# Kernel tuning notes

Measured on AMD Instinct MI355X. Metric: run time of the kernel, lower is better.

Reference implementation:

```python
import jax, jax.numpy as jnp
import numpy as np

LN_EPS = 1e-5


def _layer_norm(x, g, b):
    m = jnp.mean(x, axis=-1, keepdims=True)
    v = jnp.mean(jnp.square(x - m), axis=-1, keepdims=True)
    return (x - m) * jax.lax.rsqrt(v + LN_EPS) * g + b


def _transition(x, g, bln, w_sw, w_ss, w_sig, b_sig, w_scale, residual):
    # TransitionBlock, eval mode (dropout = identity)
    x_in = x
    x = _layer_norm(x, g, bln)
    b = jax.nn.silu(x @ w_sw.T) * (x @ w_ss.T)
    y = jax.nn.sigmoid(x @ w_sig.T + b_sig) * (b @ w_scale.T)
    return x_in + y if residual else y


def setup_inputs() -> dict:
    N, E = 1000000, 100000
    F_DIM, A_DIM, H_DIM, HEADS = 64, 128, 256, 4
    D_IN = F_DIM + A_DIM
    key = jax.random.key(0)
    ks = jax.random.split(key, 16)
    s = 0.02
    inp = {
        'v_equivariant': jax.random.normal(ks[0], (N, 3), jnp.float32),
        'v_atom_features': jax.random.normal(ks[1], (N, A_DIM), jnp.float32),
        'edge_group_idx': jnp.sort(jax.random.randint(ks[2], (N,), 0, E)).astype(jnp.int32),
        'num_edges': E,
        'fourier_w': jax.random.normal(ks[3], (F_DIM,), jnp.float32),
        'fourier_b': jax.random.normal(ks[4], (F_DIM,), jnp.float32),
        # TransitionBlock 1 (input 192 -> 256, no residual)
        'tb1_ln_g': jnp.ones((D_IN,), jnp.float32),
        'tb1_ln_b': jnp.zeros((D_IN,), jnp.float32),
        'tb1_w_sw': jax.random.normal(ks[5], (H_DIM, D_IN), jnp.float32) * s,
        'tb1_w_ss': jax.random.normal(ks[6], (H_DIM, D_IN), jnp.float32) * s,
        'tb1_w_sig': jax.random.normal(ks[7], (H_DIM, D_IN), jnp.float32) * s,
        'tb1_b_sig': jnp.full((H_DIM,), -2.0, jnp.float32),
        'tb1_w_scale': jax.random.normal(ks[8], (H_DIM, H_DIM), jnp.float32) * s,
        # TransitionBlock 2 (256 -> 256, residual)
        'tb2_ln_g': jnp.ones((H_DIM,), jnp.float32),
        'tb2_ln_b': jnp.zeros((H_DIM,), jnp.float32),
        'tb2_w_sw': jax.random.normal(ks[9], (H_DIM, H_DIM), jnp.float32) * s,
        'tb2_w_ss': jax.random.normal(ks[10], (H_DIM, H_DIM), jnp.float32) * s,
        'tb2_w_sig': jax.random.normal(ks[11], (H_DIM, H_DIM), jnp.float32) * s,
        'tb2_b_sig': jnp.full((H_DIM,), -2.0, jnp.float32),
        'tb2_w_scale': jax.random.normal(ks[12], (H_DIM, H_DIM), jnp.float32) * s,
        # final linear 256 -> num_heads
        'out_w': jax.random.normal(ks[13], (HEADS, H_DIM), jnp.float32) * s,
        'out_b': jnp.zeros((HEADS,), jnp.float32),
    }
    return inp


def reference(v_equivariant, v_atom_features, edge_group_idx, num_edges,
              fourier_w, fourier_b,
              tb1_ln_g, tb1_ln_b, tb1_w_sw, tb1_w_ss, tb1_w_sig, tb1_b_sig, tb1_w_scale,
              tb2_ln_g, tb2_ln_b, tb2_w_sw, tb2_w_ss, tb2_w_sig, tb2_b_sig, tb2_w_scale,
              out_w, out_b):
    # Fourier embedding of vector norms: [N] -> [N, F_DIM]
    v_norms = jnp.linalg.norm(v_equivariant, axis=-1)
    f_dist = jnp.cos(2.0 * jnp.pi * (v_norms[..., None] * fourier_w + fourier_b))
    x = jnp.concatenate([f_dist, v_atom_features], axis=-1)  # [N, 192]
    x = _transition(x, tb1_ln_g, tb1_ln_b, tb1_w_sw, tb1_w_ss, tb1_w_sig, tb1_b_sig, tb1_w_scale, residual=False)
    x = _transition(x, tb2_ln_g, tb2_ln_b, tb2_w_sw, tb2_w_ss, tb2_w_sig, tb2_b_sig, tb2_w_scale, residual=True)
    scores = x @ out_w.T + out_b  # [N, H]
    # scatter_softmax over edge groups (per head)
    smax = jax.ops.segment_max(scores, edge_group_idx, num_segments=num_edges)
    e = jnp.exp(scores - smax[edge_group_idx])
    ssum = jax.ops.segment_sum(e, edge_group_idx, num_segments=num_edges)
    alphas = e / ssum[edge_group_idx]  # [N, H]
    # weighted scatter-sum pooling of 3-vectors per head
    v_weighted = v_equivariant[:, None, :] * alphas[..., None]  # [N, H, 3]
    v_pooled = jax.ops.segment_sum(v_weighted, edge_group_idx, num_segments=num_edges)
    return v_pooled.reshape(num_edges, -1)  # [E, H*3]
```

## Files before the change

kernel.cpp:

```cpp
#include <hip/hip_runtime.h>
#include <math.h>

#define DIN   192
#define HD    256
#define ROWS  64
#define THREADS 256
#define LSTR  256

typedef __bf16 bf16_t;
typedef bf16_t bf16x8 __attribute__((ext_vector_type(8)));
typedef unsigned short u16x8 __attribute__((ext_vector_type(8)));
typedef float  f32x16 __attribute__((ext_vector_type(16)));

static __device__ __forceinline__ f32x16 mfma32(bf16x8 a, bf16x8 b, f32x16 c) {
  return __builtin_amdgcn_mfma_f32_32x32x16_bf16(a, b, c, 0, 0, 0);
}
static __device__ __forceinline__ unsigned short f2bfu(float f) {
  bf16_t h = (bf16_t)f; unsigned short u; __builtin_memcpy(&u, &h, 2); return u;
}
static __device__ __forceinline__ float bfu2f(unsigned short u) {
  unsigned x = ((unsigned)u) << 16; float f; __builtin_memcpy(&f, &x, 4); return f;
}
static __device__ __forceinline__ unsigned pk2(float a, float b) {
  return (unsigned)f2bfu(a) | ((unsigned)f2bfu(b) << 16);
}
static __device__ __forceinline__ float lo16(unsigned u) { return bfu2f((unsigned short)(u & 0xffff)); }
static __device__ __forceinline__ float hi16(unsigned u) { return bfu2f((unsigned short)(u >> 16)); }
static __device__ __forceinline__ float sigm(float x) {
  return __builtin_amdgcn_rcpf(1.f + __expf(-x));
}
static __device__ __forceinline__ int lidx(int row, int col) {
  return row * LSTR + (col ^ ((row & 7) << 3));
}
static __device__ __forceinline__ int crow(int r, int kg) {
  return (r & 3) + 8 * (r >> 2) + 4 * kg;
}

#define OFF_WSW1 0
#define OFF_WSS1 49152
#define OFF_WSG1 98304
#define OFF_WSC1 147456
#define OFF_WSW2 212992
#define OFF_WSS2 278528
#define OFF_WSG2 344064
#define OFF_WSC2 409600
#define OFF_WOUT 475136
#define NGRP_REORD 59392
#define NGRP_ALL   60416

__global__ void iab_wconv_kernel(const float* __restrict__ a0, const float* __restrict__ a1,
                                 const float* __restrict__ a2, const float* __restrict__ a3,
                                 const float* __restrict__ a4, const float* __restrict__ a5,
                                 const float* __restrict__ a6, const float* __restrict__ a7,
                                 const float* __restrict__ a8, unsigned short* __restrict__ out)
{
  const int i = blockIdx.x * 256 + threadIdx.x;
  if (i >= NGRP_ALL) return;
  if (i >= NGRP_REORD) {
    const int g  = i - NGRP_REORD;
    const int ks = g >> 6;
    const int ln = g & 63;
    const int col = ln & 31;
    const int kg  = ln >> 5;
    #pragma unroll
    for (int j = 0; j < 8; ++j) {
      const float vv = (col < 4) ? a8[col * 256 + ks * 16 + kg * 8 + j] : 0.f;
      out[OFF_WOUT + (size_t)g * 8 + j] = f2bfu(vv);
    }
    return;
  }
  const float* src; int off, Kd, g;
  if      (i < 6144)  { src = a0; off = OFF_WSW1; Kd = 192; g = i; }
  else if (i < 12288) { src = a1; off = OFF_WSS1; Kd = 192; g = i - 6144; }
  else if (i < 18432) { src = a2; off = OFF_WSG1; Kd = 192; g = i - 12288; }
  else if (i < 26624) { src = a3; off = OFF_WSC1; Kd = 256; g = i - 18432; }
  else if (i < 34816) { src = a4; off = OFF_WSW2; Kd = 256; g = i - 26624; }
  else if (i < 43008) { src = a5; off = OFF_WSS2; Kd = 256; g = i - 34816; }
  else if (i < 51200) { src = a6; off = OFF_WSG2; Kd = 256; g = i - 43008; }
  else                { src = a7; off = OFF_WSC2; Kd = 256; g = i - 51200; }
  const int KS   = Kd >> 4;
  const int tile = g / (KS * 64);
  const int rem  = g - tile * (KS * 64);
  const int ks   = rem >> 6;
  const int ln   = rem & 63;
  const float* sp = src + (size_t)(tile * 32 + (ln & 31)) * Kd + ks * 16 + (ln >> 5) * 8;
  #pragma unroll
  for (int j = 0; j < 8; ++j) out[off + (size_t)g * 8 + j] = f2bfu(sp[j]);
}

template<int KS>
static __device__ __forceinline__ void bgphase(const unsigned short* __restrict__ Wsw,
                                               const unsigned short* __restrict__ Wss,
                                               const unsigned short* __restrict__ Wsg,
                                               const unsigned short* __restrict__ sIn,
                                               unsigned short* __restrict__ sOut,
                                               int l31, int kg, int xr, int ocol, float bias,
                                               unsigned (&sg0)[8], unsigned (&sg1)[8])
{
  f32x16 u0{}, u1{}, s0{}, s1{}, g0{}, g1{};
  #pragma unroll 2
  for (int ks = 0; ks < KS; ++ks) {
    const bf16x8 wa = *(const bf16x8*)(Wsw + ks * 512);
    const bf16x8 wb = *(const bf16x8*)(Wss + ks * 512);
    const bf16x8 wg = *(const bf16x8*)(Wsg + ks * 512);
    const int off = ((ks * 16) + kg * 8) ^ xr;
    const bf16x8 A0 = *(const bf16x8*)(sIn + l31 * LSTR + off);
    const bf16x8 A1 = *(const bf16x8*)(sIn + (32 + l31) * LSTR + off);
    u0 = mfma32(A0, wa, u0); u1 = mfma32(A1, wa, u1);
    s0 = mfma32(A0, wb, s0); s1 = mfma32(A1, wb, s1);
    g0 = mfma32(A0, wg, g0); g1 = mfma32(A1, wg, g1);
  }
  #pragma unroll
  for (int i = 0; i < 16; ++i) {
    const float x0 = u0[i];
    const float x1 = u1[i];
    sOut[lidx(crow(i, kg),      ocol)] = f2bfu(x0 * sigm(x0) * s0[i]);
    sOut[lidx(32 + crow(i, kg), ocol)] = f2bfu(x1 * sigm(x1) * s1[i]);
  }
  #pragma unroll
  for (int p = 0; p < 8; ++p) {
    sg0[p] = pk2(sigm(g0[2*p] + bias), sigm(g0[2*p+1] + bias));
    sg1[p] = pk2(sigm(g1[2*p] + bias), sigm(g1[2*p+1] + bias));
  }
}

template<int RES>
static __device__ __forceinline__ void scphase(const unsigned short* __restrict__ Wc,
                                               const unsigned short* __restrict__ sBin,
                                               unsigned short* __restrict__ sAout,
                                               int l31, int kg, int xr, int ocol,
                                               const unsigned (&sg0)[8], const unsigned (&sg1)[8],
                                               unsigned (&x0)[8], unsigned (&x1)[8])
{
  f32x16 c0{}, c1{};
  #pragma unroll 4
  for (int ks = 0; ks < 16; ++ks) {
    const bf16x8 wv = *(const bf16x8*)(Wc + ks * 512);
    const int off = ((ks * 16) + kg * 8) ^ xr;
    const bf16x8 A0 = *(const bf16x8*)(sBin + l31 * LSTR + off);
    const bf16x8 A1 = *(const bf16x8*)(sBin + (32 + l31) * LSTR + off);
    c0 = mfma32(A0, wv, c0);
    c1 = mfma32(A1, wv, c1);
  }
  #pragma unroll
  for (int p = 0; p < 8; ++p) {
    const float ya0 = lo16(sg0[p]) * c0[2*p],  ya1 = hi16(sg0[p]) * c0[2*p+1];
    const float yb0 = lo16(sg1[p]) * c1[2*p],  yb1 = hi16(sg1[p]) * c1[2*p+1];
    if (RES) {
      x0[p] = pk2(lo16(x0[p]) + ya0, hi16(x0[p]) + ya1);
      x1[p] = pk2(lo16(x1[p]) + yb0, hi16(x1[p]) + yb1);
    } else {
      x0[p] = pk2(ya0, ya1);
      x1[p] = pk2(yb0, yb1);
    }
    const int r0 = crow(2 * p, kg);
    sAout[lidx(r0,          ocol)] = (unsigned short)(x0[p] & 0xffff);
    sAout[lidx(r0 + 1,      ocol)] = (unsigned short)(x0[p] >> 16);
    sAout[lidx(32 + r0,     ocol)] = (unsigned short)(x1[p] & 0xffff);
    sAout[lidx(32 + r0 + 1, ocol)] = (unsigned short)(x1[p] >> 16);
  }
}

#define LNACC(P) { \
  float e_; \
  e_ = bfu2f(P[0]); s += e_; sq += e_ * e_; \
  e_ = bfu2f(P[1]); s += e_; sq += e_ * e_; \
  e_ = bfu2f(P[2]); s += e_; sq += e_ * e_; \
  e_ = bfu2f(P[3]); s += e_; sq += e_ * e_; \
  e_ = bfu2f(P[4]); s += e_; sq += e_ * e_; \
  e_ = bfu2f(P[5]); s += e_; sq += e_ * e_; \
  e_ = bfu2f(P[6]); s += e_; sq += e_ * e_; \
  e_ = bfu2f(P[7]); s += e_; sq += e_ * e_; }

#define LNNORM(P, GPTR, BPTR, BASE) { \
  const int base_ = (BASE); \
  const float4 ga_ = *(const float4*)((GPTR) + base_); \
  const float4 gb_ = *(const float4*)((GPTR) + base_ + 4); \
  const float4 oa_ = *(const float4*)((BPTR) + base_); \
  const float4 ob_ = *(const float4*)((BPTR) + base_ + 4); \
  u16x8 q_; \
  q_[0] = f2bfu((bfu2f(P[0]) - mean) * rstd * ga_.x + oa_.x); \
  q_[1] = f2bfu((bfu2f(P[1]) - mean) * rstd * ga_.y + oa_.y); \
  q_[2] = f2bfu((bfu2f(P[2]) - mean) * rstd * ga_.z + oa_.z); \
  q_[3] = f2bfu((bfu2f(P[3]) - mean) * rstd * ga_.w + oa_.w); \
  q_[4] = f2bfu((bfu2f(P[4]) - mean) * rstd * gb_.x + ob_.x); \
  q_[5] = f2bfu((bfu2f(P[5]) - mean) * rstd * gb_.y + ob_.y); \
  q_[6] = f2bfu((bfu2f(P[6]) - mean) * rstd * gb_.z + ob_.z); \
  q_[7] = f2bfu((bfu2f(P[7]) - mean) * rstd * gb_.w + ob_.w); \
  *(u16x8*)(sA + r * LSTR + (base_ ^ xrr)) = q_; }

__global__ __launch_bounds__(THREADS, 2)
void iab_rows_mfma(
    const float* __restrict__ v, const float* __restrict__ af,
    const float* __restrict__ fw, const float* __restrict__ fb,
    const float* __restrict__ ln1g, const float* __restrict__ ln1b,
    const float* __restrict__ bsig1,
    const float* __restrict__ ln2g, const float* __restrict__ ln2b,
    const float* __restrict__ bsig2,
    const float* __restrict__ outb,
    const unsigned short* __restrict__ wc,
    float* __restrict__ scores, int N)
{
  __shared__ __align__(16) unsigned short sA[ROWS * LSTR];
  __shared__ __align__(16) unsigned short sB[ROWS * LSTR];

  const int t    = threadIdx.x;
  const int w    = t >> 6;
  const int lane = t & 63;
  const int l31  = lane & 31;
  const int kg   = lane >> 5;
  const int xr   = (lane & 7) << 3;
  const int row0 = blockIdx.x * ROWS;
  const int oc0  = w * 64 + l31;
  const int oc1  = oc0 + 32;
  const int T0   = w * 2;
  const int T1   = w * 2 + 1;
  const int lb   = lane * 8;

  #pragma unroll 1
  for (int it = 0; it < 2; ++it) {
    const int r   = (t >> 3) + it * 32;
    const int sub = t & 7;
    const int g   = row0 + r;
    const int xrr = (r & 7) << 3;
    float s = 0.f, sq = 0.f;
    u16x8 p0, p1 = {}, p2 = {};
    {
      float vx = 0.f, vy = 0.f, vz = 0.f;
      if (g < N) {
        vx = v[3 * (size_t)g + 0];
        vy = v[3 * (size_t)g + 1];
        vz = v[3 * (size_t)g + 2];
      }
      const float nrm = sqrtf(vx * vx + vy * vy + vz * vz);
      const float4 fwa = *(const float4*)(fw + sub * 8);
      const float4 fwb = *(const float4*)(fw + sub * 8 + 4);
      const float4 fba = *(const float4*)(fb + sub * 8);
      const float4 fbb = *(const float4*)(fb + sub * 8 + 4);
      const float e0 = __cosf(6.283185307179586f * (nrm * fwa.x + fba.x));
      const float e1 = __cosf(6.283185307179586f * (nrm * fwa.y + fba.y));
      const float e2 = __cosf(6.283185307179586f * (nrm * fwa.z + fba.z));
      const float e3 = __cosf(6.283185307179586f * (nrm * fwa.w + fba.w));
      const float e4 = __cosf(6.283185307179586f * (nrm * fwb.x + fbb.x));
      const float e5 = __cosf(6.283185307179586f * (nrm * fwb.y + fbb.y));
      const float e6 = __cosf(6.283185307179586f * (nrm * fwb.z + fbb.z));
      const float e7 = __cosf(6.283185307179586f * (nrm * fwb.w + fbb.w));
      s  += e0 + e1 + e2 + e3 + e4 + e5 + e6 + e7;
      sq += e0*e0 + e1*e1 + e2*e2 + e3*e3 + e4*e4 + e5*e5 + e6*e6 + e7*e7;
      p0[0] = f2bfu(e0); p0[1] = f2bfu(e1); p0[2] = f2bfu(e2); p0[3] = f2bfu(e3);
      p0[4] = f2bfu(e4); p0[5] = f2bfu(e5); p0[6] = f2bfu(e6); p0[7] = f2bfu(e7);
    }
    if (g < N) {
      const float* ap = af + (size_t)g * 128 + sub * 8;
      {
        const float4 a0 = *(const float4*)(ap);
        const float4 a1 = *(const float4*)(ap + 4);
        s  += a0.x + a0.y + a0.z + a0.w + a1.x + a1.y + a1.z + a1.w;
        sq += a0.x*a0.x + a0.y*a0.y + a0.z*a0.z + a0.w*a0.w
            + a1.x*a1.x + a1.y*a1.y + a1.z*a1.z + a1.w*a1.w;
        p1[0] = f2bfu(a0.x); p1[1] = f2bfu(a0.y); p1[2] = f2bfu(a0.z); p1[3] = f2bfu(a0.w);
        p1[4] = f2bfu(a1.x); p1[5] = f2bfu(a1.y); p1[6] = f2bfu(a1.z); p1[7] = f2bfu(a1.w);
      }
      {
        const float4 a2 = *(const float4*)(ap + 64);
        const float4 a3 = *(const float4*)(ap + 68);
        s  += a2.x + a2.y + a2.z + a2.w + a3.x + a3.y + a3.z + a3.w;
        sq += a2.x*a2.x + a2.y*a2.y + a2.z*a2.z + a2.w*a2.w
            + a3.x*a3.x + a3.y*a3.y + a3.z*a3.z + a3.w*a3.w;
        p2[0] = f2bfu(a2.x); p2[1] = f2bfu(a2.y); p2[2] = f2bfu(a2.z); p2[3] = f2bfu(a2.w);
        p2[4] = f2bfu(a3.x); p2[5] = f2bfu(a3.y); p2[6] = f2bfu(a3.z); p2[7] = f2bfu(a3.w);
      }
    }
    #pragma unroll
    for (int o = 1; o < 8; o <<= 1) {
      s  += __shfl_xor(s,  o);
      sq += __shfl_xor(sq, o);
    }
    const float mean = s * (1.f / 192.f);
    const float var  = fmaxf(sq * (1.f / 192.f) - mean * mean, 0.f);
    const float rstd = rsqrtf(var + 1e-5f);
    LNNORM(p0, ln1g, ln1b, sub * 8);
    LNNORM(p1, ln1g, ln1b, 64 + sub * 8);
    LNNORM(p2, ln1g, ln1b, 128 + sub * 8);
  }
  __syncthreads();

  unsigned xT0M0[8], xT0M1[8], xT1M0[8], xT1M1[8];
  unsigned gT0M0[8], gT0M1[8], gT1M0[8], gT1M1[8];

  bgphase<12>(wc + OFF_WSW1 + T0 * 12 * 512 + lb,
              wc + OFF_WSS1 + T0 * 12 * 512 + lb,
              wc + OFF_WSG1 + T0 * 12 * 512 + lb,
              sA, sB, l31, kg, xr, oc0, bsig1[oc0], gT0M0, gT0M1);
  __builtin_amdgcn_sched_barrier(0);
  bgphase<12>(wc + OFF_WSW1 + T1 * 12 * 512 + lb,
              wc + OFF_WSS1 + T1 * 12 * 512 + lb,
              wc + OFF_WSG1 + T1 * 12 * 512 + lb,
              sA, sB, l31, kg, xr, oc1, bsig1[oc1], gT1M0, gT1M1);
  __syncthreads();

  scphase<0>(wc + OFF_WSC1 + T0 * 16 * 512 + lb, sB, sA,
             l31, kg, xr, oc0, gT0M0, gT0M1, xT0M0, xT0M1);
  __builtin_amdgcn_sched_barrier(0);
  scphase<0>(wc + OFF_WSC1 + T1 * 16 * 512 + lb, sB, sA,
             l31, kg, xr, oc1, gT1M0, gT1M1, xT1M0, xT1M1);
  __syncthreads();

  #pragma unroll 1
  for (int it = 0; it < 2; ++it) {
    const int r   = (t >> 3) + it * 32;
    const int sub = t & 7;
    const int xrr = (r & 7) << 3;
    const u16x8 rv0 = *(const u16x8*)(sA + r * LSTR + ((sub * 32 +  0) ^ xrr));
    const u16x8 rv1 = *(const u16x8*)(sA + r * LSTR + ((sub * 32 +  8) ^ xrr));
    const u16x8 rv2 = *(const u16x8*)(sA + r * LSTR + ((sub * 32 + 16) ^ xrr));
    const u16x8 rv3 = *(const u16x8*)(sA + r * LSTR + ((sub * 32 + 24) ^ xrr));
    float s = 0.f, sq = 0.f;
    LNACC(rv0);
    LNACC(rv1);
    LNACC(rv2);
    LNACC(rv3);
    #pragma unroll
    for (int o = 1; o < 8; o <<= 1) {
      s  += __shfl_xor(s,  o);
      sq += __shfl_xor(sq, o);
    }
    const float mean = s * (1.f / 256.f);
    const float var  = fmaxf(sq * (1.f / 256.f) - mean * mean, 0.f);
    const float rstd = rsqrtf(var + 1e-5f);
    LNNORM(rv0, ln2g, ln2b, sub * 32 +  0);
    LNNORM(rv1, ln2g, ln2b, sub * 32 +  8);
    LNNORM(rv2, ln2g, ln2b, sub * 32 + 16);
    LNNORM(rv3, ln2g, ln2b, sub * 32 + 24);
  }
  __syncthreads();

  bgphase<16>(wc + OFF_WSW2 + T0 * 16 * 512 + lb,
              wc + OFF_WSS2 + T0 * 16 * 512 + lb,
              wc + OFF_WSG2 + T0 * 16 * 512 + lb,
              sA, sB, l31, kg, xr, oc0, bsig2[oc0], gT0M0, gT0M1);
  __builtin_amdgcn_sched_barrier(0);
  bgphase<16>(wc + OFF_WSW2 + T1 * 16 * 512 + lb,
              wc + OFF_WSS2 + T1 * 16 * 512 + lb,
              wc + OFF_WSG2 + T1 * 16 * 512 + lb,
              sA, sB, l31, kg, xr, oc1, bsig2[oc1], gT1M0, gT1M1);
  __syncthreads();

  scphase<1>(wc + OFF_WSC2 + T0 * 16 * 512 + lb, sB, sA,
             l31, kg, xr, oc0, gT0M0, gT0M1, xT0M0, xT0M1);
  __builtin_amdgcn_sched_barrier(0);
  scphase<1>(wc + OFF_WSC2 + T1 * 16 * 512 + lb, sB, sA,
             l31, kg, xr, oc1, gT1M0, gT1M1, xT1M0, xT1M1);
  __syncthreads();

  if (w < 2) {
    const unsigned short* WtF = wc + OFF_WOUT + (size_t)lane * 8;
    f32x16 c{};
    #pragma unroll 4
    for (int ks = 0; ks < 16; ++ks) {
      const bf16x8 wf = *(const bf16x8*)(WtF + ks * 512);
      const bf16x8 A  = *(const bf16x8*)(sA + (w * 32 + l31) * LSTR + (((ks * 16) + kg * 8) ^ xr));
      c = mfma32(A, wf, c);
    }
    if (l31 < 4) {
      const float bias = outb[l31];
      #pragma unroll
      for (int i = 0; i < 16; ++i) {
        const int g = row0 + w * 32 + crow(i, kg);
        if (g < N) scores[(size_t)g * 4 + l31] = c[i] + bias;
      }
    }
  }
}

__device__ __forceinline__ int iab_lower_bound(const int* __restrict__ a, int n, int key)
{
  int lo = 0, hi = n;
  while (lo < hi) {
    const int mid = (lo + hi) >> 1;
    if (a[mid] < key) lo = mid + 1; else hi = mid;
  }
  return lo;
}

__global__ __launch_bounds__(256)
void iab_segpool_kernel(const float* __restrict__ scores,
                        const float* __restrict__ v,
                        const int* __restrict__ gidx,
                        float* __restrict__ out, int N, int E)
{
  const int seg  = blockIdx.x * 4 + (threadIdx.x >> 6);
  const int lane = threadIdx.x & 63;
  if (seg >= E) return;

  const int lo = iab_lower_bound(gidx, N, seg);
  const int hi = iab_lower_bound(gidx, N, seg + 1);

  const int h  = lane & 3;
  const int ro = lane >> 2;

  float m = -INFINITY;
  for (int base = lo; base < hi; base += 16) {
    const int r = base + ro;
    if (r < hi) m = fmaxf(m, scores[(size_t)r * 4 + h]);
  }
  #pragma unroll
  for (int o = 4; o < 64; o <<= 1) m = fmaxf(m, __shfl_xor(m, o));

  float ssum = 0.f, w0 = 0.f, w1 = 0.f, w2 = 0.f;
  for (int base = lo; base < hi; base += 16) {
    const int r = base + ro;
    if (r < hi) {
      const float e = expf(scores[(size_t)r * 4 + h] - m);
      ssum += e;
      w0 += e * v[3 * (size_t)r + 0];
      w1 += e * v[3 * (size_t)r + 1];
      w2 += e * v[3 * (size_t)r + 2];
    }
  }
  #pragma unroll
  for (int o = 4; o < 64; o <<= 1) {
    ssum += __shfl_xor(ssum, o);
    w0   += __shfl_xor(w0, o);
    w1   += __shfl_xor(w1, o);
    w2   += __shfl_xor(w2, o);
  }

  if (ro == 0) {
    const float inv = (hi > lo) ? (1.f / ssum) : 0.f;
    out[(size_t)seg * 12 + h * 3 + 0] = w0 * inv;
    out[(size_t)seg * 12 + h * 3 + 1] = w1 * inv;
    out[(size_t)seg * 12 + h * 3 + 2] = w2 * inv;
  }
}

extern "C" void kernel_launch(void* const* d_in, const int* in_sizes, int n_in,
                              void* d_out, int out_size, void* d_ws, size_t ws_size,
                              hipStream_t stream)
{
  const float* v     = (const float*)d_in[0];
  const float* af    = (const float*)d_in[1];
  const int*   gidx  = (const int*)  d_in[2];
  const float* fw    = (const float*)d_in[4];
  const float* fb    = (const float*)d_in[5];
  const float* ln1g  = (const float*)d_in[6];
  const float* ln1b  = (const float*)d_in[7];
  const float* wsw1  = (const float*)d_in[8];
  const float* wss1  = (const float*)d_in[9];
  const float* wsig1 = (const float*)d_in[10];
  const float* bsig1 = (const float*)d_in[11];
  const float* wsc1  = (const float*)d_in[12];
  const float* ln2g  = (const float*)d_in[13];
  const float* ln2b  = (const float*)d_in[14];
  const float* wsw2  = (const float*)d_in[15];
  const float* wss2  = (const float*)d_in[16];
  const float* wsig2 = (const float*)d_in[17];
  const float* bsig2 = (const float*)d_in[18];
  const float* wsc2  = (const float*)d_in[19];
  const float* outw  = (const float*)d_in[20];
  const float* outb  = (const float*)d_in[21];

  const int N = in_sizes[0] / 3;
  const int E = out_size / 12;

  float* scores = (float*)d_ws;
  unsigned short* wcv = (unsigned short*)((char*)d_ws + (size_t)N * 4 * sizeof(float));

  hipLaunchKernelGGL(iab_wconv_kernel, dim3((NGRP_ALL + 255) / 256), dim3(256), 0, stream,
                     wsw1, wss1, wsig1, wsc1, wsw2, wss2, wsig2, wsc2, outw, wcv);

  hipLaunchKernelGGL(iab_rows_mfma, dim3((N + ROWS - 1) / ROWS), dim3(THREADS), 0, stream,
                     v, af, fw, fb, ln1g, ln1b, bsig1, ln2g, ln2b, bsig2, outb,
                     wcv, scores, N);

  hipLaunchKernelGGL(iab_segpool_kernel, dim3((E + 3) / 4), dim3(256), 0, stream,
                     scores, v, gidx, (float*)d_out, N, E);
}
```

Baseline: 2.417 ms.

## Move sigmoid-gate GEMM from first phase into scale phase to cut live registers

The sigmoid-gate projection is taken out of the swish/linear phase and computed at the start of the scale phase instead, reading the LN input still held in sA. Results are kept in registers and written back to sA only after an extra barrier, because sA is now read during that phase. This shortens the first phase to four accumulators and drops the packed gate registers carried across phases, aiming to reduce register pressure and raise occupancy. The cost is an additional __syncthreads per transition block and a longer second phase.

Result: faster. 2.080 ms (-14.0%).

```diff
diff --git a/kernel.cpp b/kernel.cpp
--- a/kernel.cpp
+++ b/kernel.cpp
@@ -89,26 +89,22 @@
 }
 
 template<int KS>
-static __device__ __forceinline__ void bgphase(const unsigned short* __restrict__ Wsw,
+static __device__ __forceinline__ void bphase2(const unsigned short* __restrict__ Wsw,
                                                const unsigned short* __restrict__ Wss,
-                                               const unsigned short* __restrict__ Wsg,
                                                const unsigned short* __restrict__ sIn,
                                                unsigned short* __restrict__ sOut,
-                                               int l31, int kg, int xr, int ocol, float bias,
-                                               unsigned (&sg0)[8], unsigned (&sg1)[8])
-{
-  f32x16 u0{}, u1{}, s0{}, s1{}, g0{}, g1{};
+                                               int l31, int kg, int xr, int ocol)
+{
+  f32x16 u0{}, u1{}, s0{}, s1{};
   #pragma unroll 2
   for (int ks = 0; ks < KS; ++ks) {
     const bf16x8 wa = *(const bf16x8*)(Wsw + ks * 512);
     const bf16x8 wb = *(const bf16x8*)(Wss + ks * 512);
-    const bf16x8 wg = *(const bf16x8*)(Wsg + ks * 512);
     const int off = ((ks * 16) + kg * 8) ^ xr;
     const bf16x8 A0 = *(const bf16x8*)(sIn + l31 * LSTR + off);
     const bf16x8 A1 = *(const bf16x8*)(sIn + (32 + l31) * LSTR + off);
     u0 = mfma32(A0, wa, u0); u1 = mfma32(A1, wa, u1);
     s0 = mfma32(A0, wb, s0); s1 = mfma32(A1, wb, s1);
-    g0 = mfma32(A0, wg, g0); g1 = mfma32(A1, wg, g1);
   }
   #pragma unroll
   for (int i = 0; i < 16; ++i) {
@@ -117,47 +113,71 @@
     sOut[lidx(crow(i, kg),      ocol)] = f2bfu(x0 * sigm(x0) * s0[i]);
     sOut[lidx(32 + crow(i, kg), ocol)] = f2bfu(x1 * sigm(x1) * s1[i]);
   }
+}
+
+template<int KSG, int RES>
+static __device__ __forceinline__ void cphase2(const unsigned short* __restrict__ Wg,
+                                               const unsigned short* __restrict__ Wc,
+                                               const unsigned short* __restrict__ sAin,
+                                               const unsigned short* __restrict__ sBin,
+                                               int l31, int kg, int xr, float bias,
+                                               unsigned (&x0)[8], unsigned (&x1)[8])
+{
+  unsigned pg0[8], pg1[8];
+  {
+    f32x16 g0{}, g1{};
+    #pragma unroll 4
+    for (int ks = 0; ks < KSG; ++ks) {
+      const bf16x8 wg = *(const bf16x8*)(Wg + ks * 512);
+      const int off = ((ks * 16) + kg * 8) ^ xr;
+      const bf16x8 A0 = *(const bf16x8*)(sAin + l31 * LSTR + off);
+      const bf16x8 A1 = *(const bf16x8*)(sAin + (32 + l31) * LSTR + off);
+      g0 = mfma32(A0, wg, g0);
+      g1 = mfma32(A1, wg, g1);
+    }
+    #pragma unroll
+    for (int p = 0; p < 8; ++p) {
+      pg0[p] = pk2(sigm(g0[2*p] + bias), sigm(g0[2*p+1] + bias));
+      pg1[p] = pk2(sigm(g1[2*p] + bias), sigm(g1[2*p+1] + bias));
+    }
+  }
+  {
+    f32x16 c0{}, c1{};
+    #pragma unroll 4
+    for (int ks = 0; ks < 16; ++ks) {
+      const bf16x8 wv = *(const bf16x8*)(Wc + ks * 512);
+      const int off = ((ks * 16) + kg * 8) ^ xr;
+      const bf16x8 A0 = *(const bf16x8*)(sBin + l31 * LSTR + off);
+      const bf16x8 A1 = *(const bf16x8*)(sBin + (32 + l31) * LSTR + off);
+      c0 = mfma32(A0, wv, c0);
+      c1 = mfma32(A1, wv, c1);
+    }
+    #pragma unroll
+    for (int p = 0; p < 8; ++p) {
+      const float ya0 = lo16(pg0[p]) * c0[2*p],  ya1 = hi16(pg0[p]) * c0[2*p+1];
+      const float yb0 = lo16(pg1[p]) * c1[2*p],  yb1 = hi16(pg1[p]) * c1[2*p+1];
+      if (RES) {
+        x0[p] = pk2(lo16(x0[p]) + ya0, hi16(x0[p]) + ya1);
+        x1[p] = pk2(lo16(x1[p]) + yb0, hi16(x1[p]) + yb1);
+      } else {
+        x0[p] = pk2(ya0, ya1);
+        x1[p] = pk2(yb0, yb1);
+      }
+    }
+  }
+}
+
+static __device__ __forceinline__ void storePk2(unsigned short* dst,
+                                                const unsigned (&x0)[8], const unsigned (&x1)[8],
+                                                int kg, int ocol)
+{
   #pragma unroll
   for (int p = 0; p < 8; ++p) {
-    sg0[p] = pk2(sigm(g0[2*p] + bias), sigm(g0[2*p+1] + bias));
-    sg1[p] = pk2(sigm(g1[2*p] + bias), sigm(g1[2*p+1] + bias));
-  }
-}
-
-template<int RES>
-static __device__ __forceinline__ void scphase(const unsigned short* __restrict__ Wc,
-                                               const unsigned short* __restrict__ sBin,
-                                               unsigned short* __restrict__ sAout,
-                                               int l31, int kg, int xr, int ocol,
-                                               const unsigned (&sg0)[8], const unsigned (&sg1)[8],
-                                               unsigned (&x0)[8], unsigned (&x1)[8])
-{
-  f32x16 c0{}, c1{};
-  #pragma unroll 4
-  for (int ks = 0; ks < 16; ++ks) {
-    const bf16x8 wv = *(const bf16x8*)(Wc + ks * 512);
-    const int off = ((ks * 16) + kg * 8) ^ xr;
-    const bf16x8 A0 = *(const bf16x8*)(sBin + l31 * LSTR + off);
-    const bf16x8 A1 = *(const bf16x8*)(sBin + (32 + l31) * LSTR + off);
-    c0 = mfma32(A0, wv, c0);
-    c1 = mfma32(A1, wv, c1);
-  }
-  #pragma unroll
-  for (int p = 0; p < 8; ++p) {
-    const float ya0 = lo16(sg0[p]) * c0[2*p],  ya1 = hi16(sg0[p]) * c0[2*p+1];
-    const float yb0 = lo16(sg1[p]) * c1[2*p],  yb1 = hi16(sg1[p]) * c1[2*p+1];
-    if (RES) {
-      x0[p] = pk2(lo16(x0[p]) + ya0, hi16(x0[p]) + ya1);
-      x1[p] = pk2(lo16(x1[p]) + yb0, hi16(x1[p]) + yb1);
-    } else {
-      x0[p] = pk2(ya0, ya1);
-      x1[p] = pk2(yb0, yb1);
-    }
     const int r0 = crow(2 * p, kg);
-    sAout[lidx(r0,          ocol)] = (unsigned short)(x0[p] & 0xffff);
-    sAout[lidx(r0 + 1,      ocol)] = (unsigned short)(x0[p] >> 16);
-    sAout[lidx(32 + r0,     ocol)] = (unsigned short)(x1[p] & 0xffff);
-    sAout[lidx(32 + r0 + 1, ocol)] = (unsigned short)(x1[p] >> 16);
+    dst[lidx(r0,          ocol)] = (unsigned short)(x0[p] & 0xffff);
+    dst[lidx(r0 + 1,      ocol)] = (unsigned short)(x0[p] >> 16);
+    dst[lidx(32 + r0,     ocol)] = (unsigned short)(x1[p] & 0xffff);
+    dst[lidx(32 + r0 + 1, ocol)] = (unsigned short)(x1[p] >> 16);
   }
 }
 
@@ -286,24 +306,25 @@
   __syncthreads();
 
   unsigned xT0M0[8], xT0M1[8], xT1M0[8], xT1M1[8];
-  unsigned gT0M0[8], gT0M1[8], gT1M0[8], gT1M1[8];
-
-  bgphase<12>(wc + OFF_WSW1 + T0 * 12 * 512 + lb,
-              wc + OFF_WSS1 + T0 * 12 * 512 + lb,
-              wc + OFF_WSG1 + T0 * 12 * 512 + lb,
-              sA, sB, l31, kg, xr, oc0, bsig1[oc0], gT0M0, gT0M1);
+
+  bphase2<12>(wc + OFF_WSW1 + T0 * 12 * 512 + lb,
+              wc + OFF_WSS1 + T0 * 12 * 512 + lb, sA, sB, l31, kg, xr, oc0);
   __builtin_amdgcn_sched_barrier(0);
-  bgphase<12>(wc + OFF_WSW1 + T1 * 12 * 512 + lb,
-              wc + OFF_WSS1 + T1 * 12 * 512 + lb,
-              wc + OFF_WSG1 + T1 * 12 * 512 + lb,
-              sA, sB, l31, kg, xr, oc1, bsig1[oc1], gT1M0, gT1M1);
-  __syncthreads();
-
-  scphase<0>(wc + OFF_WSC1 + T0 * 16 * 512 + lb, sB, sA,
-             l31, kg, xr, oc0, gT0M0, gT0M1, xT0M0, xT0M1);
+  bphase2<12>(wc + OFF_WSW1 + T1 * 12 * 512 + lb,
+              wc + OFF_WSS1 + T1 * 12 * 512 + lb, sA, sB, l31, kg, xr, oc1);
+  __syncthreads();
+
+  cphase2<12, 0>(wc + OFF_WSG1 + T0 * 12 * 512 + lb,
+                 wc + OFF_WSC1 + T0 * 16 * 512 + lb,
+                 sA, sB, l31, kg, xr, bsig1[oc0], xT0M0, xT0M1);
   __builtin_amdgcn_sched_barrier(0);
-  scphase<0>(wc + OFF_WSC1 + T1 * 16 * 512 + lb, sB, sA,
-             l31, kg, xr, oc1, gT1M0, gT1M1, xT1M0, xT1M1);
+  cphase2<12, 0>(wc + OFF_WSG1 + T1 * 12 * 512 + lb,
+                 wc + OFF_WSC1 + T1 * 16 * 512 + lb,
+                 sA, sB, l31, kg, xr, bsig1[oc1], xT1M0, xT1M1);
+  __syncthreads();
+
+  storePk2(sA, xT0M0, xT0M1, kg, oc0);
+  storePk2(sA, xT1M0, xT1M1, kg, oc1);
   __syncthreads();
 
   #pragma unroll 1
@@ -335,22 +356,24 @@
   }
   __syncthreads();
 
-  bgphase<16>(wc + OFF_WSW2 + T0 * 16 * 512 + lb,
-              wc + OFF_WSS2 + T0 * 16 * 512 + lb,
-              wc + OFF_WSG2 + T0 * 16 * 512 + lb,
-              sA, sB, l31, kg, xr, oc0, bsig2[oc0], gT0M0, gT0M1);
+  bphase2<16>(wc + OFF_WSW2 + T0 * 16 * 512 + lb,
+              wc + OFF_WSS2 + T0 * 16 * 512 + lb, sA, sB, l31, kg, xr, oc0);
   __builtin_amdgcn_sched_barrier(0);
-  bgphase<16>(wc + OFF_WSW2 + T1 * 16 * 512 + lb,
-              wc + OFF_WSS2 + T1 * 16 * 512 + lb,
-              wc + OFF_WSG2 + T1 * 16 * 512 + lb,
-              sA, sB, l31, kg, xr, oc1, bsig2[oc1], gT1M0, gT1M1);
-  __syncthreads();
-
-  scphase<1>(wc + OFF_WSC2 + T0 * 16 * 512 + lb, sB, sA,
-             l31, kg, xr, oc0, gT0M0, gT0M1, xT0M0, xT0M1);
+  bphase2<16>(wc + OFF_WSW2 + T1 * 16 * 512 + lb,
+              wc + OFF_WSS2 + T1 * 16 * 512 + lb, sA, sB, l31, kg, xr, oc1);
+  __syncthreads();
+
+  cphase2<16, 1>(wc + OFF_WSG2 + T0 * 16 * 512 + lb,
+                 wc + OFF_WSC2 + T0 * 16 * 512 + lb,
+                 sA, sB, l31, kg, xr, bsig2[oc0], xT0M0, xT0M1);
   __builtin_amdgcn_sched_barrier(0);
-  scphase<1>(wc + OFF_WSC2 + T1 * 16 * 512 + lb, sB, sA,
-             l31, kg, xr, oc1, gT1M0, gT1M1, xT1M0, xT1M1);
+  cphase2<16, 1>(wc + OFF_WSG2 + T1 * 16 * 512 + lb,
+                 wc + OFF_WSC2 + T1 * 16 * 512 + lb,
+                 sA, sB, l31, kg, xr, bsig2[oc1], xT1M0, xT1M1);
+  __syncthreads();
+
+  storePk2(sA, xT0M0, xT0M1, kg, oc0);
+  storePk2(sA, xT1M0, xT1M1, kg, oc1);
   __syncthreads();
 
   if (w < 2) {
```
